# Kernel tuning notes

Hardware: AMD Instinct MI355X
Metric: run time of the kernel (lower is better)

The kernel has to match this reference:

```python
import jax, jax.numpy as jnp
import numpy as np

N_NODES = 50000
N_EDGES = 800000
IN_CH = 64
OUT_CH = 64
PRIOR_VAR = 1.0


def setup_inputs() -> dict:
    key = jax.random.key(0)
    ks = jax.random.split(key, 10)
    mean = jax.random.normal(ks[0], (N_NODES, IN_CH), dtype=jnp.float32)
    std = jax.random.uniform(ks[1], (N_NODES, IN_CH), dtype=jnp.float32)
    edge_index = jax.random.randint(ks[2], (2, N_EDGES), 0, N_NODES, dtype=jnp.int32)
    edge_weight = jax.random.uniform(ks[3], (N_EDGES,), dtype=jnp.float32)
    # Bayesian GCN parameters (xavier-ish mu, log_sigma init -3.0) for mean- and std-branches
    scale = float(np.sqrt(6.0 / (IN_CH + OUT_CH)))
    mu_mean = jax.random.uniform(ks[4], (IN_CH, OUT_CH), minval=-scale, maxval=scale, dtype=jnp.float32)
    log_sigma_mean = jnp.full((IN_CH, OUT_CH), -3.0, dtype=jnp.float32)
    mu_std = jax.random.uniform(ks[5], (IN_CH, OUT_CH), minval=-scale, maxval=scale, dtype=jnp.float32)
    log_sigma_std = jnp.full((IN_CH, OUT_CH), -3.0, dtype=jnp.float32)
    # reparameterization noise (drawn once so reference is deterministic)
    eps_mean = jax.random.normal(ks[6], (IN_CH, OUT_CH), dtype=jnp.float32)
    eps_std = jax.random.normal(ks[7], (IN_CH, OUT_CH), dtype=jnp.float32)
    return {
        "mean": mean, "std": std, "edge_index": edge_index, "edge_weight": edge_weight,
        "mu_mean": mu_mean, "log_sigma_mean": log_sigma_mean, "eps_mean": eps_mean,
        "mu_std": mu_std, "log_sigma_std": log_sigma_std, "eps_std": eps_std,
    }


def _gcn_propagate(x, weight, edge_index, edge_weight):
    # support = x @ W; then gather src rows, scale by edge_weight, scatter-add to dst
    support = jnp.matmul(x, weight)                      # [N, out]
    src, dst = edge_index[0], edge_index[1]
    msg = edge_weight[:, None] * support[src]            # [E, out]
    return jax.ops.segment_sum(msg, dst, num_segments=N_NODES)


def _kl(mu, log_sigma):
    pv = PRIOR_VAR
    kl = 0.5 * (jnp.exp(2.0 * log_sigma) / pv + mu ** 2 / pv
                - 2.0 * log_sigma - jnp.log(jnp.asarray(pv, mu.dtype)) - 1.0)
    return kl.sum()


def reference(mean, std, edge_index, edge_weight,
              mu_mean, log_sigma_mean, eps_mean,
              mu_std, log_sigma_std, eps_std):
    # mean branch
    w_mean = mu_mean + eps_mean * jnp.exp(log_sigma_mean)
    new_mean = _gcn_propagate(mean, w_mean, edge_index, edge_weight)
    kl_mean = _kl(mu_mean, log_sigma_mean)
    # std branch operates on variance with squared edge weights
    var = std ** 2
    w_std = mu_std + eps_std * jnp.exp(log_sigma_std)
    new_log_var = _gcn_propagate(var, w_std, edge_index, edge_weight ** 2)
    kl_std = _kl(mu_std, log_sigma_std)
    new_std = jnp.sqrt(jnp.exp(new_log_var) + 1e-6)
    total_kl = kl_mean + kl_std
    return (new_mean, new_std, total_kl)
```

## Files before the change

### kernel.cpp

```cpp
#include <hip/hip_runtime.h>

#define N_NODES 50000
#define N_EDGES 800000
#define CH 64
#define OUT_OFF_STD (N_NODES * CH)
#define OUT_OFF_KL  (2 * N_NODES * CH)
#define CAP 64
#define GEMM_BLOCKS 782
#define FILL_BLOCKS 3125

typedef __attribute__((ext_vector_type(8))) short short8;
typedef __attribute__((ext_vector_type(4))) float f32x4;

__device__ __forceinline__ int rl_i(unsigned v, int lane) {
    return __builtin_amdgcn_readlane((int)v, lane);
}
__device__ __forceinline__ unsigned f2bf(float f) {
    unsigned u = __float_as_uint(f);
    return (u + 0x7fffu + ((u >> 16) & 1u)) >> 16;
}

__global__ __launch_bounds__(256) void wkl_kernel(
    const float* __restrict__ mu_m, const float* __restrict__ ls_m,
    const float* __restrict__ eps_m,
    const float* __restrict__ mu_s, const float* __restrict__ ls_s,
    const float* __restrict__ eps_s,
    unsigned short* __restrict__ fragBm, unsigned short* __restrict__ fragBv,
    float* __restrict__ kl_out)
{
    float kl = 0.0f;
    for (int f = threadIdx.x; f < CH * CH; f += 256) {
        int j = f & 7, l = (f >> 3) & 63, ch = f >> 9;
        int k = (ch & 1) * 32 + ((l >> 4) & 3) * 8 + j;
        int n = (ch >> 1) * 16 + (l & 15);
        int idx = k * CH + n;
        float mu = mu_m[idx], ls = ls_m[idx];
        fragBm[f] = (unsigned short)f2bf(mu + eps_m[idx] * expf(ls));
        kl += 0.5f * (expf(2.0f * ls) + mu * mu - 2.0f * ls - 1.0f);
        mu = mu_s[idx]; ls = ls_s[idx];
        fragBv[f] = (unsigned short)f2bf(mu + eps_s[idx] * expf(ls));
        kl += 0.5f * (expf(2.0f * ls) + mu * mu - 2.0f * ls - 1.0f);
    }
    for (int off = 32; off > 0; off >>= 1)
        kl += __shfl_down(kl, off, 64);
    __shared__ float red[4];
    if ((threadIdx.x & 63) == 0) red[threadIdx.x >> 6] = kl;
    __syncthreads();
    if (threadIdx.x == 0)
        kl_out[0] = red[0] + red[1] + red[2] + red[3];
}

__global__ __launch_bounds__(256) void gemfill_kernel(
    const float* __restrict__ mean, const float* __restrict__ stdv,
    const unsigned short* __restrict__ fragBm,
    const unsigned short* __restrict__ fragBv,
    const int* __restrict__ ei, const float* __restrict__ ew,
    int* __restrict__ cur, uint2* __restrict__ bins,
    unsigned* __restrict__ sup)
{
    const int tid = threadIdx.x;

    if (blockIdx.x >= GEMM_BLOCKS) {
        int e = (blockIdx.x - GEMM_BLOCKS) * 256 + tid;
        int src = ei[e];
        int dst = ei[N_EDGES + e];
        float w = ew[e];
        int slot = atomicAdd(&cur[dst], 1);
        if (slot < CAP)
            bins[(size_t)dst * CAP + slot] =
                make_uint2((unsigned)src, __float_as_uint(w));
        return;
    }

    const int lane = tid & 63, wave = tid >> 6;
    const int row0 = blockIdx.x * 64 + wave * 16;
    if (row0 >= N_NODES) return;

    const int m = lane & 15;
    const int q = (lane >> 4) & 3;
    const float* mrow = mean + (size_t)(row0 + m) * CH + q * 8;
    const float* srow = stdv + (size_t)(row0 + m) * CH + q * 8;

    short8 aM[2], aV[2];
#pragma unroll
    for (int h = 0; h < 2; ++h) {
        float4 x0 = *(const float4*)(mrow + h * 32);
        float4 x1 = *(const float4*)(mrow + h * 32 + 4);
        float4 s0 = *(const float4*)(srow + h * 32);
        float4 s1 = *(const float4*)(srow + h * 32 + 4);
        aM[h][0] = (short)f2bf(x0.x); aM[h][1] = (short)f2bf(x0.y);
        aM[h][2] = (short)f2bf(x0.z); aM[h][3] = (short)f2bf(x0.w);
        aM[h][4] = (short)f2bf(x1.x); aM[h][5] = (short)f2bf(x1.y);
        aM[h][6] = (short)f2bf(x1.z); aM[h][7] = (short)f2bf(x1.w);
        aV[h][0] = (short)f2bf(s0.x * s0.x); aV[h][1] = (short)f2bf(s0.y * s0.y);
        aV[h][2] = (short)f2bf(s0.z * s0.z); aV[h][3] = (short)f2bf(s0.w * s0.w);
        aV[h][4] = (short)f2bf(s1.x * s1.x); aV[h][5] = (short)f2bf(s1.y * s1.y);
        aV[h][6] = (short)f2bf(s1.z * s1.z); aV[h][7] = (short)f2bf(s1.w * s1.w);
    }

    f32x4 accM[4], accV[4];
#pragma unroll
    for (int c = 0; c < 4; ++c) {
        accM[c] = (f32x4)0.0f;
        accV[c] = (f32x4)0.0f;
    }
#pragma unroll
    for (int c = 0; c < 4; ++c) {
#pragma unroll
        for (int h = 0; h < 2; ++h) {
            short8 bm = *(const short8*)(fragBm + ((c * 2 + h) * 64 + lane) * 8);
            short8 bv = *(const short8*)(fragBv + ((c * 2 + h) * 64 + lane) * 8);
            accM[c] = __builtin_amdgcn_mfma_f32_16x16x32_bf16(aM[h], bm, accM[c], 0, 0, 0);
            accV[c] = __builtin_amdgcn_mfma_f32_16x16x32_bf16(aV[h], bv, accV[c], 0, 0, 0);
        }
    }

    const int rg = lane >> 4;
#pragma unroll
    for (int c = 0; c < 4; ++c) {
#pragma unroll
        for (int r = 0; r < 4; ++r) {
            int node = row0 + rg * 4 + r;
            sup[(size_t)node * CH + c * 16 + m] =
                f2bf(accM[c][r]) | (f2bf(accV[c][r]) << 16);
        }
    }
}

__global__ __launch_bounds__(256) void gather_kernel(
    const int* __restrict__ cur, const uint2* __restrict__ bins,
    const unsigned* __restrict__ sup, float* __restrict__ out)
{
    const int wave = threadIdx.x >> 6;
    const int col = threadIdx.x & 63;
    const int n = blockIdx.x * 4 + wave;

    int cnt = cur[n];
    if (cnt > CAP) cnt = CAP;
    uint2 p = make_uint2(0u, 0u);
    if (col < cnt) p = bins[(size_t)n * CAP + col];

    float accM = 0.0f, accV = 0.0f;
    for (int i = 0; i < cnt; i += 4) {
        const bool v1 = (i + 1 < cnt), v2 = (i + 2 < cnt), v3 = (i + 3 < cnt);
        int s0 = rl_i(p.x, i);
        int s1 = v1 ? rl_i(p.x, i + 1) : 0;
        int s2 = v2 ? rl_i(p.x, i + 2) : 0;
        int s3 = v3 ? rl_i(p.x, i + 3) : 0;
        float w0 = __uint_as_float((unsigned)rl_i(p.y, i));
        float w1 = v1 ? __uint_as_float((unsigned)rl_i(p.y, i + 1)) : 0.0f;
        float w2 = v2 ? __uint_as_float((unsigned)rl_i(p.y, i + 2)) : 0.0f;
        float w3 = v3 ? __uint_as_float((unsigned)rl_i(p.y, i + 3)) : 0.0f;
        unsigned q0 = sup[(size_t)s0 * CH + col];
        unsigned q1 = sup[(size_t)s1 * CH + col];
        unsigned q2 = sup[(size_t)s2 * CH + col];
        unsigned q3 = sup[(size_t)s3 * CH + col];
        float m0 = __uint_as_float(q0 << 16), vv0 = __uint_as_float(q0 & 0xFFFF0000u);
        float m1 = __uint_as_float(q1 << 16), vv1 = __uint_as_float(q1 & 0xFFFF0000u);
        float m2 = __uint_as_float(q2 << 16), vv2 = __uint_as_float(q2 & 0xFFFF0000u);
        float m3 = __uint_as_float(q3 << 16), vv3 = __uint_as_float(q3 & 0xFFFF0000u);
        accM += w0 * m0 + w1 * m1;
        accM += w2 * m2 + w3 * m3;
        accV += (w0 * w0) * vv0 + (w1 * w1) * vv1;
        accV += (w2 * w2) * vv2 + (w3 * w3) * vv3;
    }
    out[(size_t)n * CH + col] = accM;
    out[OUT_OFF_STD + (size_t)n * CH + col] = sqrtf(expf(accV) + 1e-6f);
}

extern "C" void kernel_launch(void* const* d_in, const int* in_sizes, int n_in,
                              void* d_out, int out_size, void* d_ws, size_t ws_size,
                              hipStream_t stream)
{
    const float* mean  = (const float*)d_in[0];
    const float* stdv  = (const float*)d_in[1];
    const int*   ei    = (const int*)d_in[2];
    const float* ew    = (const float*)d_in[3];
    const float* mu_m  = (const float*)d_in[4];
    const float* ls_m  = (const float*)d_in[5];
    const float* eps_m = (const float*)d_in[6];
    const float* mu_s  = (const float*)d_in[7];
    const float* ls_s  = (const float*)d_in[8];
    const float* eps_s = (const float*)d_in[9];

    float* out = (float*)d_out;
    int*            cur    = (int*)d_ws;
    unsigned*       sup    = (unsigned*)(cur + N_NODES);
    uint2*          bins   = (uint2*)(sup + (size_t)N_NODES * CH);
    unsigned short* fragBm = (unsigned short*)(bins + (size_t)N_NODES * CAP);
    unsigned short* fragBv = fragBm + CH * CH;

    hipMemsetAsync(cur, 0, N_NODES * sizeof(int), stream);

    wkl_kernel<<<1, 256, 0, stream>>>(mu_m, ls_m, eps_m, mu_s, ls_s, eps_s,
                                      fragBm, fragBv, out + OUT_OFF_KL);
    gemfill_kernel<<<GEMM_BLOCKS + FILL_BLOCKS, 256, 0, stream>>>(
        mean, stdv, fragBm, fragBv, ei, ew, cur, bins, sup);
    gather_kernel<<<N_NODES / 4, 256, 0, stream>>>(cur, bins, sup, out);
}
```

Baseline: 205.3 us.

## Partition edge binning and gather by destination group for XCD locality

The fill phase now splits destination nodes into 8 groups. Each block scans a 2048-edge chunk and only bins edges whose destination falls in its group. Because blockIdx mod 8 matches a group, the atomics and bin writes for a node range should stay on one XCD's L2, and the gather kernel uses the same group mapping so it reads those bins locally. The costs are that every edge index is read 8 times, and fill blocks are now scheduled before the GEMM blocks. The gather loop is also unrolled to 8 loads in flight, and the weight-fragment kernel now stages weights through shared memory for coalesced reads.

```diff
diff --git a/kernel.cpp b/kernel.cpp
--- a/kernel.cpp
+++ b/kernel.cpp
@@ -6,8 +6,14 @@
 #define OUT_OFF_STD (N_NODES * CH)
 #define OUT_OFF_KL  (2 * N_NODES * CH)
 #define CAP 64
+
+#define NGRP 8
+#define NPG 6250
+#define FILL_CHUNK 2048
+#define FILL_CHUNKS 391
+#define FILL_BLOCKS (NGRP * FILL_CHUNKS)
 #define GEMM_BLOCKS 782
-#define FILL_BLOCKS 3125
+#define GATHER_CHUNKS 1563
 
 typedef __attribute__((ext_vector_type(8))) short short8;
 typedef __attribute__((ext_vector_type(4))) float f32x4;
@@ -28,18 +34,24 @@
     unsigned short* __restrict__ fragBm, unsigned short* __restrict__ fragBv,
     float* __restrict__ kl_out)
 {
+    __shared__ unsigned short Wm[CH * CH];
+    __shared__ unsigned short Wv[CH * CH];
     float kl = 0.0f;
+    for (int i = threadIdx.x; i < CH * CH; i += 256) {
+        float mu = mu_m[i], ls = ls_m[i];
+        Wm[i] = (unsigned short)f2bf(mu + eps_m[i] * expf(ls));
+        kl += 0.5f * (expf(2.0f * ls) + mu * mu - 2.0f * ls - 1.0f);
+        mu = mu_s[i]; ls = ls_s[i];
+        Wv[i] = (unsigned short)f2bf(mu + eps_s[i] * expf(ls));
+        kl += 0.5f * (expf(2.0f * ls) + mu * mu - 2.0f * ls - 1.0f);
+    }
+    __syncthreads();
     for (int f = threadIdx.x; f < CH * CH; f += 256) {
         int j = f & 7, l = (f >> 3) & 63, ch = f >> 9;
         int k = (ch & 1) * 32 + ((l >> 4) & 3) * 8 + j;
         int n = (ch >> 1) * 16 + (l & 15);
-        int idx = k * CH + n;
-        float mu = mu_m[idx], ls = ls_m[idx];
-        fragBm[f] = (unsigned short)f2bf(mu + eps_m[idx] * expf(ls));
-        kl += 0.5f * (expf(2.0f * ls) + mu * mu - 2.0f * ls - 1.0f);
-        mu = mu_s[idx]; ls = ls_s[idx];
-        fragBv[f] = (unsigned short)f2bf(mu + eps_s[idx] * expf(ls));
-        kl += 0.5f * (expf(2.0f * ls) + mu * mu - 2.0f * ls - 1.0f);
+        fragBm[f] = Wm[k * CH + n];
+        fragBv[f] = Wv[k * CH + n];
     }
     for (int off = 32; off > 0; off >>= 1)
         kl += __shfl_down(kl, off, 64);
@@ -60,20 +72,31 @@
 {
     const int tid = threadIdx.x;
 
-    if (blockIdx.x >= GEMM_BLOCKS) {
-        int e = (blockIdx.x - GEMM_BLOCKS) * 256 + tid;
-        int src = ei[e];
-        int dst = ei[N_EDGES + e];
-        float w = ew[e];
-        int slot = atomicAdd(&cur[dst], 1);
-        if (slot < CAP)
-            bins[(size_t)dst * CAP + slot] =
-                make_uint2((unsigned)src, __float_as_uint(w));
+    if (blockIdx.x < FILL_BLOCKS) {
+        const int g = blockIdx.x & (NGRP - 1);
+        const int chunk = blockIdx.x >> 3;
+        const int base = chunk * FILL_CHUNK;
+        const int lo = g * NPG;
+#pragma unroll
+        for (int r = 0; r < FILL_CHUNK / 256; ++r) {
+            int e = base + r * 256 + tid;
+            if (e < N_EDGES) {
+                int dst = ei[N_EDGES + e];
+                if ((unsigned)(dst - lo) < (unsigned)NPG) {
+                    int src = ei[e];
+                    float w = ew[e];
+                    int slot = atomicAdd(&cur[dst], 1);
+                    if (slot < CAP)
+                        bins[(size_t)dst * CAP + slot] =
+                            make_uint2((unsigned)src, __float_as_uint(w));
+                }
+            }
+        }
         return;
     }
 
     const int lane = tid & 63, wave = tid >> 6;
-    const int row0 = blockIdx.x * 64 + wave * 16;
+    const int row0 = (blockIdx.x - FILL_BLOCKS) * 64 + wave * 16;
     if (row0 >= N_NODES) return;
 
     const int m = lane & 15;
@@ -131,9 +154,13 @@
     const int* __restrict__ cur, const uint2* __restrict__ bins,
     const unsigned* __restrict__ sup, float* __restrict__ out)
 {
+    const int g = blockIdx.x & (NGRP - 1);
+    const int cid = blockIdx.x >> 3;
     const int wave = threadIdx.x >> 6;
     const int col = threadIdx.x & 63;
-    const int n = blockIdx.x * 4 + wave;
+    const int loc = cid * 4 + wave;
+    if (loc >= NPG) return;
+    const int n = g * NPG + loc;
 
     int cnt = cur[n];
     if (cnt > CAP) cnt = CAP;
@@ -141,28 +168,26 @@
     if (col < cnt) p = bins[(size_t)n * CAP + col];
 
     float accM = 0.0f, accV = 0.0f;
-    for (int i = 0; i < cnt; i += 4) {
-        const bool v1 = (i + 1 < cnt), v2 = (i + 2 < cnt), v3 = (i + 3 < cnt);
-        int s0 = rl_i(p.x, i);
-        int s1 = v1 ? rl_i(p.x, i + 1) : 0;
-        int s2 = v2 ? rl_i(p.x, i + 2) : 0;
-        int s3 = v3 ? rl_i(p.x, i + 3) : 0;
-        float w0 = __uint_as_float((unsigned)rl_i(p.y, i));
-        float w1 = v1 ? __uint_as_float((unsigned)rl_i(p.y, i + 1)) : 0.0f;
-        float w2 = v2 ? __uint_as_float((unsigned)rl_i(p.y, i + 2)) : 0.0f;
-        float w3 = v3 ? __uint_as_float((unsigned)rl_i(p.y, i + 3)) : 0.0f;
-        unsigned q0 = sup[(size_t)s0 * CH + col];
-        unsigned q1 = sup[(size_t)s1 * CH + col];
-        unsigned q2 = sup[(size_t)s2 * CH + col];
-        unsigned q3 = sup[(size_t)s3 * CH + col];
-        float m0 = __uint_as_float(q0 << 16), vv0 = __uint_as_float(q0 & 0xFFFF0000u);
-        float m1 = __uint_as_float(q1 << 16), vv1 = __uint_as_float(q1 & 0xFFFF0000u);
-        float m2 = __uint_as_float(q2 << 16), vv2 = __uint_as_float(q2 & 0xFFFF0000u);
-        float m3 = __uint_as_float(q3 << 16), vv3 = __uint_as_float(q3 & 0xFFFF0000u);
-        accM += w0 * m0 + w1 * m1;
-        accM += w2 * m2 + w3 * m3;
-        accV += (w0 * w0) * vv0 + (w1 * w1) * vv1;
-        accV += (w2 * w2) * vv2 + (w3 * w3) * vv3;
+    for (int i = 0; i < cnt; i += 8) {
+        int   s[8];
+        float w[8];
+#pragma unroll
+        for (int t = 0; t < 8; ++t) {
+            bool v = (i + t < cnt);
+            s[t] = v ? rl_i(p.x, i + t) : 0;
+            w[t] = v ? __uint_as_float((unsigned)rl_i(p.y, i + t)) : 0.0f;
+        }
+        unsigned q[8];
+#pragma unroll
+        for (int t = 0; t < 8; ++t)
+            q[t] = sup[(size_t)s[t] * CH + col];
+#pragma unroll
+        for (int t = 0; t < 8; ++t) {
+            float mm = __uint_as_float(q[t] << 16);
+            float vv = __uint_as_float(q[t] & 0xFFFF0000u);
+            accM += w[t] * mm;
+            accV += (w[t] * w[t]) * vv;
+        }
     }
     out[(size_t)n * CH + col] = accM;
     out[OUT_OFF_STD + (size_t)n * CH + col] = sqrtf(expf(accV) + 1e-6f);
@@ -179,8 +204,8 @@
     const float* mu_m  = (const float*)d_in[4];
     const float* ls_m  = (const float*)d_in[5];
     const float* eps_m = (const float*)d_in[6];
+    const float* ls_s  = (const float*)d_in[8];
     const float* mu_s  = (const float*)d_in[7];
-    const float* ls_s  = (const float*)d_in[8];
     const float* eps_s = (const float*)d_in[9];
 
     float* out = (float*)d_out;
@@ -194,7 +219,7 @@
 
     wkl_kernel<<<1, 256, 0, stream>>>(mu_m, ls_m, eps_m, mu_s, ls_s, eps_s,
                                       fragBm, fragBv, out + OUT_OFF_KL);
-    gemfill_kernel<<<GEMM_BLOCKS + FILL_BLOCKS, 256, 0, stream>>>(
+    gemfill_kernel<<<FILL_BLOCKS + GEMM_BLOCKS, 256, 0, stream>>>(
         mean, stdv, fragBm, fragBv, ei, ew, cur, bins, sup);
-    gather_kernel<<<N_NODES / 4, 256, 0, stream>>>(cur, bins, sup, out);
-}
+    gather_kernel<<<NGRP * GATHER_CHUNKS, 256, 0, stream>>>(cur, bins, sup, out);
+}
```

Measured after the change: 190.3 us. 7.3% less time.
